# Performance work log

Hardware: AMD Instinct MI355X
Metric: run time of the kernel (lower is better)

## Reference

```python
import jax, jax.numpy as jnp
import numpy as np

N = 50000      # num nodes
E = 800000     # num edges
F_IN = 100     # input features (ogbn-products)
HID = 128      # hidden_dim (per-head out_channels)
H = 2          # heads
OUT = 47       # num classes
NEG_SLOPE = 0.2


def setup_inputs() -> dict:
    key = jax.random.key(0)
    ks = jax.random.split(key, 14)
    def glorot(k, shape, fan):
        return jax.random.normal(k, shape, jnp.float32) * (1.0 / np.sqrt(fan))
    x = jax.random.normal(ks[0], (N, F_IN), jnp.float32)
    edge_index = jax.random.randint(ks[1], (2, E), 0, N)
    # GAT layer 0: lin_l (= lin_r, shared) weight [H*HID, F_IN], attention vecs [H, HID]
    W0 = glorot(ks[2], (H * HID, F_IN), F_IN)
    b0 = jnp.zeros((H * HID,), jnp.float32)
    attl0 = glorot(ks[3], (H, HID), HID)
    attr0 = glorot(ks[4], (H, HID), HID)
    # GAT layer 1: input dim H*HID
    W1 = glorot(ks[5], (H * HID, H * HID), H * HID)
    b1 = jnp.zeros((H * HID,), jnp.float32)
    attl1 = glorot(ks[6], (H, HID), HID)
    attr1 = glorot(ks[7], (H, HID), HID)
    # post_mp: Linear(H*HID -> HID), Linear(HID -> OUT)
    Wp1 = glorot(ks[8], (HID, H * HID), H * HID)
    bp1 = jnp.zeros((HID,), jnp.float32)
    Wp2 = glorot(ks[9], (OUT, HID), HID)
    bp2 = jnp.zeros((OUT,), jnp.float32)
    return dict(x=x, edge_index=edge_index, W0=W0, b0=b0, attl0=attl0, attr0=attr0,
                W1=W1, b1=b1, attl1=attl1, attr1=attr1,
                Wp1=Wp1, bp1=bp1, Wp2=Wp2, bp2=bp2)


def gat_layer(x, W, b, att_l, att_r, src, dst):
    # shared lin_l == lin_r in the source
    h = (x @ W.T + b).reshape(-1, H, HID)          # [N, H, C]
    alpha_l = jnp.einsum('nhc,hc->nh', h, att_l)   # per-node left scores
    alpha_r = jnp.einsum('nhc,hc->nh', h, att_r)   # per-node right scores
    e = jax.nn.leaky_relu(alpha_l[src] + alpha_r[dst], NEG_SLOPE)  # [E, H]
    # segment softmax over edges grouped by destination node
    emax = jax.ops.segment_max(e, dst, num_segments=N)             # [N, H]
    ee = jnp.exp(e - emax[dst])
    denom = jax.ops.segment_sum(ee, dst, num_segments=N)           # [N, H]
    a = ee / denom[dst]                                            # [E, H]
    msg = a[:, :, None] * h[src]                                   # [E, H, C]
    out = jax.ops.segment_sum(msg, dst, num_segments=N)            # [N, H, C]
    return out.reshape(-1, H * HID)


def reference(x, edge_index, W0, b0, attl0, attr0, W1, b1, attl1, attr1, Wp1, bp1, Wp2, bp2):
    src, dst = edge_index[0], edge_index[1]
    x = jax.nn.relu(gat_layer(x, W0, b0, attl0, attr0, src, dst))
    x = jax.nn.relu(gat_layer(x, W1, b1, attl1, attr1, src, dst))
    h = x @ Wp1.T + bp1           # dropout p=0.0 -> identity
    logits = h @ Wp2.T + bp2
    return jax.nn.log_softmax(logits, axis=1)
```

## Files before the change

kernel.cpp:

```cpp
#include <hip/hip_runtime.h>
#include <math.h>

#define N_NODES 50000
#define E_EDGES 800000
#define F_IN 100
#define HID 128
#define HEADS 2
#define OUT_C 47
#define HH (HEADS*HID)
#define MPAD 50176
#define SLOTS 64
#define NGEMM 1568
#define NEB 3136

typedef float floatx4 __attribute__((ext_vector_type(4)));
typedef float float2v __attribute__((ext_vector_type(2)));
typedef short short8 __attribute__((ext_vector_type(8)));

__device__ inline ushort bf16round(float v) {
    unsigned u = __float_as_uint(v);
    return (ushort)((u + 0x7FFFu + ((u >> 16) & 1u)) >> 16);
}

__device__ __forceinline__ void gl_lds16(const void* g, void* l) {
    __builtin_amdgcn_global_load_lds(
        (const __attribute__((address_space(1))) unsigned int*)g,
        (__attribute__((address_space(3))) unsigned int*)l, 16, 0, 0);
}

__device__ __forceinline__ void epi2h(
    const floatx4* acc,
    const float* __restrict__ bias,
    const float* __restrict__ attl, const float* __restrict__ attr,
    ushort* __restrict__ Hb, float* __restrict__ al, float* __restrict__ ar,
    int m0, int wave, int lane)
{
    const int quad = lane >> 4, l16 = lane & 15;
#pragma unroll
    for (int h = 0; h < 2; h++) {
        float bias_r[8], att_l[8], att_r[8];
#pragma unroll
        for (int sn = 0; sn < 8; sn++) {
            int ai = h * 128 + sn * 16 + l16;
            bias_r[sn] = bias[ai];
            att_l[sn] = attl[ai];
            att_r[sn] = attr[ai];
        }
#pragma unroll
        for (int r = 0; r < 4; r++) {
            int gm = m0 + wave * 16 + quad * 4 + r;
            float suml = 0.f, sumr = 0.f;
#pragma unroll
            for (int sn = 0; sn < 8; sn++) {
                float v = acc[h * 8 + sn][r] + bias_r[sn];
                suml += v * att_l[sn];
                sumr += v * att_r[sn];
                if (gm < N_NODES) {
                    int gn = h * 128 + sn * 16 + l16;
                    Hb[(size_t)gm * 256 + gn] = bf16round(v);
                }
            }
#pragma unroll
            for (int off = 1; off < 16; off <<= 1) {
                suml += __shfl_xor(suml, off);
                sumr += __shfl_xor(sumr, off);
            }
            if (l16 == 0 && gm < N_NODES) {
                al[gm * HEADS + h] = suml;
                ar[gm * HEADS + h] = sumr;
            }
        }
    }
}

__global__ void prep(int* __restrict__ deg,
                     const float* __restrict__ W0, const float* __restrict__ W1,
                     const float* __restrict__ Wp1, const float* __restrict__ Wp2,
                     const float* __restrict__ bp1, const float* __restrict__ bp2,
                     ushort* __restrict__ W0b, ushort* __restrict__ W1b,
                     ushort* __restrict__ Wcb, float* __restrict__ bcb) {
    const int c0 = 256 * 32;
    const int c1 = c0 + 16384;
    const int c2 = c1 + 16384;
    const int c3 = c2 + 64;
    int i = blockIdx.x * 256 + threadIdx.x;
    if (i < N_NODES) deg[i] = 0;
    if (i >= c3) return;
    if (i < c0) {
        int row = i >> 5, kc = (i & 31) * 4;
        float4 v = make_float4(0.f, 0.f, 0.f, 0.f);
        if (kc < F_IN) v = *(const float4*)(W0 + (size_t)row * F_IN + kc);
        ushort4 r;
        r.x = bf16round(v.x); r.y = bf16round(v.y);
        r.z = bf16round(v.z); r.w = bf16round(v.w);
        *(ushort4*)(W0b + (size_t)row * 128 + kc) = r;
    } else if (i < c1) {
        int j = i - c0;
        float4 v = *(const float4*)(W1 + (size_t)j * 4);
        ushort4 r;
        r.x = bf16round(v.x); r.y = bf16round(v.y);
        r.z = bf16round(v.z); r.w = bf16round(v.w);
        *(ushort4*)(W1b + (size_t)j * 4) = r;
    } else if (i < c2) {
        int j = i - c1;
        int o = j >> 8, k = j & 255;
        float acc = 0.f;
        if (o < OUT_C) {
            for (int jj = 0; jj < HID; jj++)
                acc += Wp2[o * HID + jj] * Wp1[(size_t)jj * HH + k];
        }
        Wcb[(size_t)o * HH + k] = bf16round(acc);
    } else {
        int o = i - c2;
        float acc = 0.f;
        if (o < OUT_C) {
            for (int jj = 0; jj < HID; jj++) acc += Wp2[o * HID + jj] * bp1[jj];
            acc += bp2[o];
        }
        bcb[o] = acc;
    }
}

__global__ __launch_bounds__(128) void gemm_l0_edges(
    const float* __restrict__ x, const ushort* __restrict__ W0b,
    const float* __restrict__ b0,
    const float* __restrict__ attl0, const float* __restrict__ attr0,
    ushort* __restrict__ hb, float* __restrict__ al, float* __restrict__ ar,
    const int* __restrict__ srcv, const int* __restrict__ dstv,
    int* __restrict__ deg, ushort* __restrict__ csr16)
{
    __shared__ ushort sA[32 * 32];
    __shared__ ushort sB[256 * 32];
    const int g = blockIdx.x;
    if (g % 3 == 0) {
        const int by = g / 3;
        const int t = threadIdx.x;
        const int wave = t >> 6, lane = t & 63;
        const int quad = lane >> 4, l16 = lane & 15;
        const int rl = lane >> 2, seg = lane & 3;
        const int m0 = by * 32;

        floatx4 acc[16];
#pragma unroll
        for (int j = 0; j < 16; j++) acc[j] = (floatx4)(0.f);

        for (int k0 = 0; k0 < 128; k0 += 32) {
#pragma unroll
            for (int rnd = 0; rnd < 2; rnd++) {
                int row = wave * 16 + (lane >> 3) + rnd * 8;
                int c4 = (lane & 7) * 4;
                int col = k0 + c4;
                int gmr = m0 + row;
                float4 v = make_float4(0.f, 0.f, 0.f, 0.f);
                if (gmr < N_NODES && col < F_IN)
                    v = *(const float4*)(x + (size_t)gmr * F_IN + col);
                ushort4 u;
                u.x = bf16round(v.x); u.y = bf16round(v.y);
                u.z = bf16round(v.z); u.w = bf16round(v.w);
                *(ushort4*)(sA + row * 32 + c4) = u;
            }
#pragma unroll
            for (int j = 0; j < 8; j++) {
                int br = wave * 128 + j * 16;
                size_t gro = (size_t)(br + rl) * 128 + k0 + seg * 8;
                gl_lds16(W0b + gro, sB + br * 32);
            }
            __syncthreads();
            short8 af = *(const short8*)(sA + (wave * 16 + l16) * 32 + quad * 8);
#pragma unroll
            for (int sn = 0; sn < 16; sn++) {
                short8 b = *(const short8*)(sB + (sn * 16 + l16) * 32 + quad * 8);
                acc[sn] = __builtin_amdgcn_mfma_f32_16x16x32_bf16(af, b, acc[sn], 0, 0, 0);
            }
            __syncthreads();
        }
        epi2h(acc, b0, attl0, attr0, hb, al, ar, m0, wave, lane);
    } else {
        const int eidx = g - g / 3 - 1;
        int e0 = eidx * 256 + threadIdx.x;
#pragma unroll
        for (int rep = 0; rep < 2; rep++) {
            int e = e0 + rep * 128;
            if (e < E_EDGES) {
                int d = dstv[e];
                int r = atomicAdd(&deg[d], 1);
                if (r < SLOTS) csr16[(size_t)d * SLOTS + r] = (ushort)srcv[e];
            }
        }
    }
}

__global__ __launch_bounds__(128) void gemm_l1(
    const ushort* __restrict__ Ab, const ushort* __restrict__ Wb,
    const float* __restrict__ bias, ushort* __restrict__ Hb,
    const float* __restrict__ attl, const float* __restrict__ attr,
    float* __restrict__ al, float* __restrict__ ar)
{
    __shared__ ushort sA[32 * 32];
    __shared__ ushort sB[256 * 32];
    const int t = threadIdx.x;
    const int wave = t >> 6, lane = t & 63;
    const int quad = lane >> 4, l16 = lane & 15;
    const int rl = lane >> 2, seg = lane & 3;
    const int m0 = blockIdx.x * 32;

    floatx4 acc[16];
#pragma unroll
    for (int j = 0; j < 16; j++) acc[j] = (floatx4)(0.f);

    for (int k0 = 0; k0 < HH; k0 += 32) {
        {
            size_t gro = (size_t)(m0 + wave * 16 + rl) * HH + k0 + seg * 8;
            gl_lds16(Ab + gro, sA + (wave * 16) * 32);
        }
#pragma unroll
        for (int j = 0; j < 8; j++) {
            int br = wave * 128 + j * 16;
            size_t gro = (size_t)(br + rl) * HH + k0 + seg * 8;
            gl_lds16(Wb + gro, sB + br * 32);
        }
        __syncthreads();
        short8 af = *(const short8*)(sA + (wave * 16 + l16) * 32 + quad * 8);
#pragma unroll
        for (int sn = 0; sn < 16; sn++) {
            short8 b = *(const short8*)(sB + (sn * 16 + l16) * 32 + quad * 8);
            acc[sn] = __builtin_amdgcn_mfma_f32_16x16x32_bf16(af, b, acc[sn], 0, 0, 0);
        }
        __syncthreads();
    }
    epi2h(acc, bias, attl, attr, Hb, al, ar, m0, wave, lane);
}

__global__ __launch_bounds__(256) void gat_aggregate(
    const ushort* __restrict__ hb, const float* __restrict__ al, const float* __restrict__ ar,
    const int* __restrict__ deg, const ushort* __restrict__ csr16,
    ushort* __restrict__ outb)
{
    const int g = blockIdx.x;
    const int xcd = g & 7;
    const int head = xcd & 1;
    const int rank = (g >> 3) * 4 + (xcd >> 1);
    const int wave = threadIdx.x >> 6;
    const int node = rank * 4 + wave;
    const int lane = threadIdx.x & 63;
    const int grp = lane >> 4, c = lane & 15;
    const int n = min(deg[node], SLOTS);
    const float ard = ar[node * HEADS + head];
    const ushort* __restrict__ hbh = hb + head * HID + c * 8;

    float dsum = 0.f;
    float2v av[4];
#pragma unroll
    for (int j = 0; j < 4; j++) av[j] = (float2v)(0.f);

    int s = 0; float w = 0.f;
    if (lane < n) {
        s = (int)csr16[(size_t)node * SLOTS + lane];
        float e = al[s * HEADS + head] + ard;
        e = fmaxf(e, 0.f) + 0.2f * fminf(e, 0.f);
        w = __expf(e);
        dsum = w;
    }
    const int nn = (n + 7) & ~7;
    for (int i = 0; i < nn; i += 8) {
        int e0 = i + grp, e1 = i + 4 + grp;
        int   s0 = __shfl(s, e0);
        float w0 = __shfl(w, e0);
        int   s1 = __shfl(s, e1);
        float w1 = __shfl(w, e1);
        uint4 q0 = *(const uint4*)(hbh + (size_t)s0 * 256);
        uint4 q1 = *(const uint4*)(hbh + (size_t)s1 * 256);
        float2v we0 = (float2v)(w0);
        float2v we1 = (float2v)(w1);
        float2v p;
        p.x = __uint_as_float(q0.x << 16); p.y = __uint_as_float(q0.x & 0xFFFF0000u);
        av[0] += we0 * p;
        p.x = __uint_as_float(q0.y << 16); p.y = __uint_as_float(q0.y & 0xFFFF0000u);
        av[1] += we0 * p;
        p.x = __uint_as_float(q0.z << 16); p.y = __uint_as_float(q0.z & 0xFFFF0000u);
        av[2] += we0 * p;
        p.x = __uint_as_float(q0.w << 16); p.y = __uint_as_float(q0.w & 0xFFFF0000u);
        av[3] += we0 * p;
        p.x = __uint_as_float(q1.x << 16); p.y = __uint_as_float(q1.x & 0xFFFF0000u);
        av[0] += we1 * p;
        p.x = __uint_as_float(q1.y << 16); p.y = __uint_as_float(q1.y & 0xFFFF0000u);
        av[1] += we1 * p;
        p.x = __uint_as_float(q1.z << 16); p.y = __uint_as_float(q1.z & 0xFFFF0000u);
        av[2] += we1 * p;
        p.x = __uint_as_float(q1.w << 16); p.y = __uint_as_float(q1.w & 0xFFFF0000u);
        av[3] += we1 * p;
    }
#pragma unroll
    for (int j = 0; j < 4; j++) {
        av[j].x += __shfl_xor(av[j].x, 16);
        av[j].y += __shfl_xor(av[j].y, 16);
        av[j].x += __shfl_xor(av[j].x, 32);
        av[j].y += __shfl_xor(av[j].y, 32);
    }
#pragma unroll
    for (int off = 32; off; off >>= 1) dsum += __shfl_xor(dsum, off);

    if (grp == 0) {
        const float inv = (n > 0) ? 1.f / dsum : 0.f;
        ushort r[8];
#pragma unroll
        for (int j = 0; j < 4; j++) {
            r[2*j]   = bf16round(fmaxf(av[j].x * inv, 0.f));
            r[2*j+1] = bf16round(fmaxf(av[j].y * inv, 0.f));
        }
        *(uint4*)(outb + (size_t)node * 256 + head * HID + c * 8) = *(uint4*)r;
    }
}

__global__ __launch_bounds__(256) void fused_post_c(
    const ushort* __restrict__ Ab,
    const ushort* __restrict__ Wcb,
    const float* __restrict__ bcb,
    float* __restrict__ out, int M)
{
    __shared__ ushort sA[64 * 32];
    __shared__ ushort sB[64 * 32];
    const int t = threadIdx.x;
    const int wave = t >> 6, lane = t & 63;
    const int quad = lane >> 4, l16 = lane & 15;
    const int rl = lane >> 2, seg = lane & 3;
    const int m0 = blockIdx.x * 64;

    floatx4 acc[4];
#pragma unroll
    for (int j = 0; j < 4; j++) acc[j] = (floatx4)(0.f);

    for (int k0 = 0; k0 < HH; k0 += 32) {
        {
            size_t gro = (size_t)(m0 + wave * 16 + rl) * HH + k0 + seg * 8;
            gl_lds16(Ab + gro, sA + (wave * 16) * 32);
        }
        {
            size_t gro = (size_t)(wave * 16 + rl) * HH + k0 + seg * 8;
            gl_lds16(Wcb + gro, sB + (wave * 16) * 32);
        }
        __syncthreads();
        short8 af = *(const short8*)(sA + (wave * 16 + l16) * 32 + quad * 8);
#pragma unroll
        for (int sn = 0; sn < 4; sn++) {
            short8 b = *(const short8*)(sB + (sn * 16 + l16) * 32 + quad * 8);
            acc[sn] = __builtin_amdgcn_mfma_f32_16x16x32_bf16(af, b, acc[sn], 0, 0, 0);
        }
        __syncthreads();
    }

    float b2[4];
#pragma unroll
    for (int sn = 0; sn < 4; sn++) {
        int n = sn * 16 + l16;
        b2[sn] = (n < OUT_C) ? bcb[n] : 0.f;
    }
#pragma unroll
    for (int r = 0; r < 4; r++) {
        float v[4];
        float m = -INFINITY;
#pragma unroll
        for (int sn = 0; sn < 4; sn++) {
            int n = sn * 16 + l16;
            float xv = (n < OUT_C) ? acc[sn][r] + b2[sn] : -INFINITY;
            v[sn] = xv;
            m = fmaxf(m, xv);
        }
#pragma unroll
        for (int off = 1; off < 16; off <<= 1) m = fmaxf(m, __shfl_xor(m, off));
        float ssum = 0.f;
#pragma unroll
        for (int sn = 0; sn < 4; sn++) {
            int n = sn * 16 + l16;
            if (n < OUT_C) ssum += __expf(v[sn] - m);
        }
#pragma unroll
        for (int off = 1; off < 16; off <<= 1) ssum += __shfl_xor(ssum, off);
        float lse = m + logf(ssum);
        int gm = m0 + wave * 16 + quad * 4 + r;
        if (gm < M) {
#pragma unroll
            for (int sn = 0; sn < 4; sn++) {
                int n = sn * 16 + l16;
                if (n < OUT_C) out[(size_t)gm * OUT_C + n] = v[sn] - lse;
            }
        }
    }
}

extern "C" void kernel_launch(void* const* d_in, const int* in_sizes, int n_in,
                              void* d_out, int out_size, void* d_ws, size_t ws_size,
                              hipStream_t stream) {
    const float* x     = (const float*)d_in[0];
    const int*   ei    = (const int*)d_in[1];
    const float* W0    = (const float*)d_in[2];
    const float* b0    = (const float*)d_in[3];
    const float* attl0 = (const float*)d_in[4];
    const float* attr0 = (const float*)d_in[5];
    const float* W1    = (const float*)d_in[6];
    const float* b1    = (const float*)d_in[7];
    const float* attl1 = (const float*)d_in[8];
    const float* attr1 = (const float*)d_in[9];
    const float* Wp1   = (const float*)d_in[10];
    const float* bp1   = (const float*)d_in[11];
    const float* Wp2   = (const float*)d_in[12];
    const float* bp2   = (const float*)d_in[13];
    float* out = (float*)d_out;

    const int Nn = N_NODES, Etot = E_EDGES;
    const int* srcv = ei;
    const int* dstv = ei + Etot;

    char* ws = (char*)d_ws;
    size_t off = 0;
    auto alloc = [&](size_t bytes) -> void* {
        void* p = ws + off;
        off = (off + bytes + 255) & ~(size_t)255;
        return p;
    };
    int*    deg    = (int*)alloc((size_t)Nn * sizeof(int));
    ushort* csr16  = (ushort*)alloc((size_t)Nn * SLOTS * 2);
    float*  al     = (float*)alloc((size_t)Nn * HEADS * sizeof(float));
    float*  ar     = (float*)alloc((size_t)Nn * HEADS * sizeof(float));
    ushort* W0b    = (ushort*)alloc((size_t)HH * 128 * 2);
    ushort* W1b    = (ushort*)alloc((size_t)HH * HH * 2);
    ushort* Wcb    = (ushort*)alloc((size_t)64 * HH * 2);
    float*  bcb    = (float*)alloc(64 * sizeof(float));
    ushort* hb     = (ushort*)alloc((size_t)MPAD * HH * 2);
    ushort* xbb    = (ushort*)alloc((size_t)MPAD * HH * 2);

    prep<<<196, 256, 0, stream>>>(deg, W0, W1, Wp1, Wp2, bp1, bp2,
                                  W0b, W1b, Wcb, bcb);

    gemm_l0_edges<<<NGEMM + NEB, 128, 0, stream>>>(
        x, W0b, b0, attl0, attr0, hb, al, ar, srcv, dstv, deg, csr16);

    gat_aggregate<<<25000, 256, 0, stream>>>(hb, al, ar, deg, csr16, xbb);

    gemm_l1<<<NGEMM, 128, 0, stream>>>(xbb, W1b, b1, hb, attl1, attr1, al, ar);

    gat_aggregate<<<25000, 256, 0, stream>>>(hb, al, ar, deg, csr16, xbb);

    fused_post_c<<<MPAD / 64, 256, 0, stream>>>(xbb, Wcb, bcb, out, Nn);
}
```

Measured before the change: 286.2 us.

## Double-buffer layer-1 GEMM with single-wave blocks and swizzled W1 layout

Rewrites the layer-1 GEMM as a single-wave block that computes 32 rows and stages the next K-slice into a second LDS buffer while the current one feeds MFMA. The __syncthreads barriers are replaced by explicit vmcnt waits. The prep kernel now writes W1 in bf16 with its 16-byte chunks XOR-swizzled by row, so the B-fragment LDS reads avoid bank conflicts. In exchange each block uses more LDS and registers (two accumulator sets), and each SIMD runs fewer waves to hide latency.

```diff
diff --git a/kernel.cpp b/kernel.cpp
--- a/kernel.cpp
+++ b/kernel.cpp
@@ -96,11 +96,14 @@
         *(ushort4*)(W0b + (size_t)row * 128 + kc) = r;
     } else if (i < c1) {
         int j = i - c0;
+        int row = j >> 6, c4 = j & 63;
+        int c16 = c4 >> 1, e8 = c4 & 1;
+        int c16s = (c16 & ~3) | ((c16 & 3) ^ (row & 3));
         float4 v = *(const float4*)(W1 + (size_t)j * 4);
         ushort4 r;
         r.x = bf16round(v.x); r.y = bf16round(v.y);
         r.z = bf16round(v.z); r.w = bf16round(v.w);
-        *(ushort4*)(W1b + (size_t)j * 4) = r;
+        *(ushort4*)(W1b + (size_t)row * 256 + c16s * 8 + e8 * 4) = r;
     } else if (i < c2) {
         int j = i - c1;
         int o = j >> 8, k = j & 255;
@@ -190,45 +193,59 @@
     }
 }
 
-__global__ __launch_bounds__(128) void gemm_l1(
-    const ushort* __restrict__ Ab, const ushort* __restrict__ Wb,
+__global__ __launch_bounds__(64) void gemm_l1_pipe(
+    const ushort* __restrict__ Ab, const ushort* __restrict__ Wswz,
     const float* __restrict__ bias, ushort* __restrict__ Hb,
     const float* __restrict__ attl, const float* __restrict__ attr,
     float* __restrict__ al, float* __restrict__ ar)
 {
-    __shared__ ushort sA[32 * 32];
-    __shared__ ushort sB[256 * 32];
-    const int t = threadIdx.x;
-    const int wave = t >> 6, lane = t & 63;
+    __shared__ __align__(16) ushort sA[2][32 * 32];
+    __shared__ __align__(16) ushort sB[2][256 * 32];
+    const int lane = threadIdx.x;
     const int quad = lane >> 4, l16 = lane & 15;
     const int rl = lane >> 2, seg = lane & 3;
     const int m0 = blockIdx.x * 32;
-
-    floatx4 acc[16];
-#pragma unroll
-    for (int j = 0; j < 16; j++) acc[j] = (floatx4)(0.f);
-
-    for (int k0 = 0; k0 < HH; k0 += 32) {
-        {
-            size_t gro = (size_t)(m0 + wave * 16 + rl) * HH + k0 + seg * 8;
-            gl_lds16(Ab + gro, sA + (wave * 16) * 32);
-        }
-#pragma unroll
-        for (int j = 0; j < 8; j++) {
-            int br = wave * 128 + j * 16;
-            size_t gro = (size_t)(br + rl) * HH + k0 + seg * 8;
-            gl_lds16(Wb + gro, sB + br * 32);
-        }
-        __syncthreads();
-        short8 af = *(const short8*)(sA + (wave * 16 + l16) * 32 + quad * 8);
+    const int bswz = ((quad ^ (l16 & 3)) << 3);
+
+    floatx4 acc[2][16];
+#pragma unroll
+    for (int s = 0; s < 2; s++)
+#pragma unroll
+        for (int j = 0; j < 16; j++) acc[s][j] = (floatx4)(0.f);
+
+    auto stage = [&](int k0, ushort* dA, ushort* dB) {
+#pragma unroll
+        for (int j = 0; j < 2; j++)
+            gl_lds16(Ab + (size_t)(m0 + j * 16 + rl) * HH + k0 + seg * 8,
+                     dA + (j * 16) * 32);
+#pragma unroll
+        for (int j = 0; j < 16; j++)
+            gl_lds16(Wswz + (size_t)(j * 16 + rl) * HH + k0 + seg * 8,
+                     dB + (j * 16) * 32);
+    };
+
+    stage(0, sA[0], sB[0]);
+#pragma unroll
+    for (int k = 0; k < 8; k++) {
+        const int cur = k & 1;
+        if (k < 7) {
+            stage((k + 1) * 32, sA[cur ^ 1], sB[cur ^ 1]);
+            asm volatile("s_waitcnt vmcnt(18)" ::: "memory");
+        } else {
+            asm volatile("s_waitcnt vmcnt(0)" ::: "memory");
+        }
+        __builtin_amdgcn_sched_barrier(0);
+        short8 af0 = *(const short8*)(&sA[cur][l16 * 32 + quad * 8]);
+        short8 af1 = *(const short8*)(&sA[cur][(16 + l16) * 32 + quad * 8]);
 #pragma unroll
         for (int sn = 0; sn < 16; sn++) {
-            short8 b = *(const short8*)(sB + (sn * 16 + l16) * 32 + quad * 8);
-            acc[sn] = __builtin_amdgcn_mfma_f32_16x16x32_bf16(af, b, acc[sn], 0, 0, 0);
-        }
-        __syncthreads();
-    }
-    epi2h(acc, bias, attl, attr, Hb, al, ar, m0, wave, lane);
+            short8 b = *(const short8*)(&sB[cur][(sn * 16 + l16) * 32 + bswz]);
+            acc[0][sn] = __builtin_amdgcn_mfma_f32_16x16x32_bf16(af0, b, acc[0][sn], 0, 0, 0);
+            acc[1][sn] = __builtin_amdgcn_mfma_f32_16x16x32_bf16(af1, b, acc[1][sn], 0, 0, 0);
+        }
+    }
+    epi2h(acc[0], bias, attl, attr, Hb, al, ar, m0, 0, lane);
+    epi2h(acc[1], bias, attl, attr, Hb, al, ar, m0, 1, lane);
 }
 
 __global__ __launch_bounds__(256) void gat_aggregate(
@@ -437,7 +454,7 @@
 
     gat_aggregate<<<25000, 256, 0, stream>>>(hb, al, ar, deg, csr16, xbb);
 
-    gemm_l1<<<NGEMM, 128, 0, stream>>>(xbb, W1b, b1, hb, attl1, attr1, al, ar);
+    gemm_l1_pipe<<<MPAD / 32, 64, 0, stream>>>(xbb, W1b, b1, hb, attl1, attr1, al, ar);
 
     gat_aggregate<<<25000, 256, 0, stream>>>(hb, al, ar, deg, csr16, xbb);
 
```

Result: no change. 290.1 us (+1.4%).
